# Performance work log

Measured on AMD Instinct MI355X. Metric: run time of the kernel, lower is better.

The kernel has to match this reference:

```python
import jax, jax.numpy as jnp
import numpy as np


def setup_inputs() -> dict:
    key = jax.random.key(0)
    ks = jax.random.split(key, 8)
    B, N, M, H = 8192, 2048, 2048, 10
    return {
        "X": jax.random.normal(ks[0], (B, N), dtype=jnp.float32),
        "weight": jax.random.normal(ks[1], (N, M), dtype=jnp.float32),
        "W1": jax.random.normal(ks[2], (3, H), dtype=jnp.float32) * 0.5,
        "b1": jax.random.normal(ks[3], (H,), dtype=jnp.float32) * 0.1,
        "W2": jax.random.normal(ks[4], (H, H), dtype=jnp.float32) * 0.3,
        "b2": jax.random.normal(ks[5], (H,), dtype=jnp.float32) * 0.1,
        "W3": jax.random.normal(ks[6], (H, 1), dtype=jnp.float32) * 0.3,
        "b3": jax.random.normal(ks[7], (1,), dtype=jnp.float32) * 0.1,
    }


def reference(X, weight, W1, b1, W2, b2, W3, b3):
    # NCA local rule, vectorized over all (i, j) cells.
    # 'forward'  = mean of column j excluding row i  (leave-one-out col mean)
    # 'backward' = mean of row i excluding column j  (leave-one-out row mean)
    n, m = weight.shape
    col_sum = jnp.sum(weight, axis=0, keepdims=True)            # [1, m]
    row_sum = jnp.sum(weight, axis=1, keepdims=True)            # [n, 1]
    fwd_mean = (col_sum - weight) / jnp.float32(n - 1)          # [n, m]
    bwd_mean = (row_sum - weight) / jnp.float32(m - 1)          # [n, m]
    feats = jnp.stack([weight, fwd_mean, bwd_mean], axis=-1)    # [n, m, 3]
    # tiny 3 -> 10 -> 10 -> 1 MLP applied per cell
    h = jax.nn.relu(feats @ W1 + b1)                            # [n, m, 10]
    h = jax.nn.relu(h @ W2 + b2)                                # [n, m, 10]
    updates = (h @ W3 + b3)[..., 0]                             # [n, m]
    new_weight = weight + updates
    # forward: softmax(X @ W)
    return jax.nn.softmax(X @ new_weight, axis=-1)
```

## Files before the change

### kernel.cpp

```cpp
#include <hip/hip_runtime.h>
#include <hip/hip_bf16.h>


typedef int int4v __attribute__((ext_vector_type(4)));
typedef int int16v __attribute__((ext_vector_type(16)));

#define GK 2048
#define NROWS 2048
#define MCOLS 2048
#define NCHUNK 16

#define CS_BLOCKS 128
#define RS_BLOCKS 2048
__global__ __launch_bounds__(256) void pre_kernel(
    const float* __restrict__ X, const float* __restrict__ W,
    signed char* __restrict__ X1, signed char* __restrict__ X2,
    float* __restrict__ sx1,
    float* __restrict__ part, float* __restrict__ rowS) {
  const int bid = blockIdx.x;
  const int tid = threadIdx.x;

  if (bid < CS_BLOCKS) {
    int chunk = bid >> 3;
    int j = (bid & 7) * 256 + tid;
    int i0 = chunk * (NROWS / NCHUNK);
    float s = 0.f;
    for (int i = i0; i < i0 + NROWS / NCHUNK; ++i) s += W[(size_t)i * MCOLS + j];
    part[(size_t)chunk * MCOLS + j] = s;
    return;
  }
  if (bid < CS_BLOCKS + RS_BLOCKS) {
    int row = bid - CS_BLOCKS;
    const float4* p = (const float4*)(W + (size_t)row * MCOLS);
    float4 a = p[tid];
    float4 b = p[tid + 256];
    float v = (a.x + a.y) + (a.z + a.w) + (b.x + b.y) + (b.z + b.w);
    __shared__ float red[256];
    red[tid] = v;
    __syncthreads();
    for (int s = 128; s > 0; s >>= 1) {
      if (tid < s) red[tid] += red[tid + s];
      __syncthreads();
    }
    if (tid == 0) rowS[row] = red[0];
    return;
  }
  {
    int row = bid - CS_BLOCKS - RS_BLOCKS;
    const float4* xr = (const float4*)(X + (size_t)row * GK);
    float4 a = xr[tid * 2];
    float4 b = xr[tid * 2 + 1];
    float xs[8] = {a.x, a.y, a.z, a.w, b.x, b.y, b.z, b.w};
    float am = 0.f;
#pragma unroll
    for (int i = 0; i < 8; ++i) am = fmaxf(am, fabsf(xs[i]));
    const int lane = tid & 63, wv = tid >> 6;
#pragma unroll
    for (int off = 32; off > 0; off >>= 1)
      am = fmaxf(am, __shfl_xor(am, off));
    __shared__ float wred[4];
    if (lane == 0) wred[wv] = am;
    __syncthreads();
    float amax = fmaxf(fmaxf(wred[0], wred[1]), fmaxf(wred[2], wred[3]));
    float s1 = amax * (1.0f / 127.0f);
    float inv = 127.0f / amax;
    int q1[8], q2[8];
#pragma unroll
    for (int i = 0; i < 8; ++i) {
      q1[i] = (int)rintf(xs[i] * inv);
      float r = xs[i] - (float)q1[i] * s1;
      q2[i] = (int)rintf(r * (254.0f * inv));
    }
    unsigned lo1 = (q1[0] & 255) | ((q1[1] & 255) << 8) | ((q1[2] & 255) << 16) | ((q1[3] & 255) << 24);
    unsigned hi1 = (q1[4] & 255) | ((q1[5] & 255) << 8) | ((q1[6] & 255) << 16) | ((q1[7] & 255) << 24);
    unsigned lo2 = (q2[0] & 255) | ((q2[1] & 255) << 8) | ((q2[2] & 255) << 16) | ((q2[3] & 255) << 24);
    unsigned hi2 = (q2[4] & 255) | ((q2[5] & 255) << 8) | ((q2[6] & 255) << 16) | ((q2[7] & 255) << 24);
    ((uint2*)(X1 + (size_t)row * GK))[tid] = make_uint2(lo1, hi1);
    ((uint2*)(X2 + (size_t)row * GK))[tid] = make_uint2(lo2, hi2);
    if (tid == 0) sx1[row] = s1;
  }
}

__global__ __launch_bounds__(256) void nca_update_kernel(
    const float* __restrict__ W, const float* __restrict__ part,
    const float* __restrict__ rowS,
    const float* __restrict__ W1, const float* __restrict__ b1,
    const float* __restrict__ W2, const float* __restrict__ b2,
    const float* __restrict__ W3, const float* __restrict__ b3,
    float* __restrict__ Wt) {
  __shared__ float sColS[32];
  __shared__ float cred[NCHUNK][33];
  __shared__ float Tf[32][33];
  const int tid = threadIdx.x;
  const int i0 = blockIdx.y * 32;
  const int j0 = blockIdx.x * 32;

  {
    int ch = tid >> 5;
    int jl = tid & 31;
    cred[ch][jl]     = part[(size_t)ch * MCOLS + j0 + jl];
    cred[ch + 8][jl] = part[(size_t)(ch + 8) * MCOLS + j0 + jl];
  }
  __syncthreads();
  if (tid < 32) {
    float s = 0.f;
#pragma unroll
    for (int c = 0; c < NCHUNK; ++c) s += cred[c][tid];
    sColS[tid] = s;
  }
  __syncthreads();

  const int r = tid >> 5;
  const int c = tid & 31;

  float w[4], fwd[4], bwd[4];
#pragma unroll
  for (int cell = 0; cell < 4; ++cell) {
    int il = r + 8 * cell;
    float wv = W[(size_t)(i0 + il) * MCOLS + j0 + c];
    w[cell] = wv;
    fwd[cell] = (sColS[c] - wv) * (1.0f / (float)(NROWS - 1));
    bwd[cell] = (rowS[i0 + il] - wv) * (1.0f / (float)(MCOLS - 1));
  }

  float h1[4][10];
#pragma unroll
  for (int o = 0; o < 10; ++o) {
    float w1a = W1[o], w1b = W1[10 + o], w1c = W1[20 + o], bb = b1[o];
#pragma unroll
    for (int cell = 0; cell < 4; ++cell) {
      float v = fmaf(w[cell], w1a, fmaf(fwd[cell], w1b, fmaf(bwd[cell], w1c, bb)));
      h1[cell][o] = fmaxf(v, 0.f);
    }
  }
  const float b3v = b3[0];
  float u[4] = {b3v, b3v, b3v, b3v};
#pragma unroll
  for (int o = 0; o < 10; ++o) {
    float h2[4];
    float bb = b2[o];
#pragma unroll
    for (int cell = 0; cell < 4; ++cell) h2[cell] = bb;
#pragma unroll
    for (int p = 0; p < 10; ++p) {
      float wv = W2[p * 10 + o];
#pragma unroll
      for (int cell = 0; cell < 4; ++cell) h2[cell] = fmaf(h1[cell][p], wv, h2[cell]);
    }
    float w3 = W3[o];
#pragma unroll
    for (int cell = 0; cell < 4; ++cell) u[cell] = fmaf(fmaxf(h2[cell], 0.f), w3, u[cell]);
  }

#pragma unroll
  for (int cell = 0; cell < 4; ++cell) {
    int il = r + 8 * cell;
    Tf[il][c] = w[cell] + u[cell];
  }
  __syncthreads();

  {
    int r2 = tid >> 4;
    int ic = (tid & 15) * 2;
#pragma unroll
    for (int half = 0; half < 2; ++half) {
      int jl = r2 + 16 * half;
      float2 v = make_float2(Tf[ic][jl], Tf[ic + 1][jl]);
      *(float2*)(&Wt[(size_t)(j0 + jl) * NROWS + i0 + ic]) = v;
    }
  }
}

__global__ __launch_bounds__(256) void bquant_kernel(
    const float* __restrict__ Wt, signed char* __restrict__ B1,
    signed char* __restrict__ B2, float* __restrict__ sw1) {
  const int row = blockIdx.x;
  const int tid = threadIdx.x;
  const float4* wr = (const float4*)(Wt + (size_t)row * GK);
  float4 a = wr[tid * 2];
  float4 b = wr[tid * 2 + 1];
  float xs[8] = {a.x, a.y, a.z, a.w, b.x, b.y, b.z, b.w};
  float am = 0.f;
#pragma unroll
  for (int i = 0; i < 8; ++i) am = fmaxf(am, fabsf(xs[i]));
  const int lane = tid & 63, wv = tid >> 6;
#pragma unroll
  for (int off = 32; off > 0; off >>= 1)
    am = fmaxf(am, __shfl_xor(am, off));
  __shared__ float wred[4];
  if (lane == 0) wred[wv] = am;
  __syncthreads();
  float amax = fmaxf(fmaxf(wred[0], wred[1]), fmaxf(wred[2], wred[3]));
  float s1 = amax * (1.0f / 127.0f);
  float inv = 127.0f / amax;
  int q1[8], q2[8];
#pragma unroll
  for (int i = 0; i < 8; ++i) {
    q1[i] = (int)rintf(xs[i] * inv);
    float r = xs[i] - (float)q1[i] * s1;
    q2[i] = (int)rintf(r * (254.0f * inv));
  }
  unsigned lo1 = (q1[0] & 255) | ((q1[1] & 255) << 8) | ((q1[2] & 255) << 16) | ((q1[3] & 255) << 24);
  unsigned hi1 = (q1[4] & 255) | ((q1[5] & 255) << 8) | ((q1[6] & 255) << 16) | ((q1[7] & 255) << 24);
  unsigned lo2 = (q2[0] & 255) | ((q2[1] & 255) << 8) | ((q2[2] & 255) << 16) | ((q2[3] & 255) << 24);
  unsigned hi2 = (q2[4] & 255) | ((q2[5] & 255) << 8) | ((q2[6] & 255) << 16) | ((q2[7] & 255) << 24);
  ((uint2*)(B1 + (size_t)row * GK))[tid] = make_uint2(lo1, hi1);
  ((uint2*)(B2 + (size_t)row * GK))[tid] = make_uint2(lo2, hi2);
  if (tid == 0) sw1[row] = s1;
}

#define BM 128
#define BN 128
#define BK 64
#define NT (GK / BK)
#define BUFSZ 32768
#define SROWSZ ((size_t)16 * GK)

__device__ __forceinline__ void glds16(const signed char* g, char* l) {
  __builtin_amdgcn_global_load_lds(
      (const __attribute__((address_space(1))) void*)g,
      (__attribute__((address_space(3))) void*)l, 16, 0, 0);
}

__device__ __forceinline__ int4v ds_read128(const char* p) {
  int4v r;
  asm volatile("ds_read_b128 %0, %1"
               : "=v"(r)
               : "v"((const __attribute__((address_space(3))) char*)p));
  return r;
}

#define MFMA_I8 __builtin_amdgcn_mfma_i32_32x32x32_i8

#define RD16(NX, rb_)                                                          \
  NX##a1[0][0] = ds_read128((rb_) + aoff[0][0]);                               \
  NX##a1[0][1] = ds_read128((rb_) + aoff[0][1]);                               \
  NX##a1[1][0] = ds_read128((rb_) + aoff[1][0]);                               \
  NX##a1[1][1] = ds_read128((rb_) + aoff[1][1]);                               \
  NX##a2[0][0] = ds_read128((rb_) + aoff[0][0] + 8192);                        \
  NX##a2[0][1] = ds_read128((rb_) + aoff[0][1] + 8192);                        \
  NX##a2[1][0] = ds_read128((rb_) + aoff[1][0] + 8192);                        \
  NX##a2[1][1] = ds_read128((rb_) + aoff[1][1] + 8192);                        \
  NX##b1[0][0] = ds_read128((rb_) + boff[0][0]);                               \
  NX##b1[0][1] = ds_read128((rb_) + boff[0][1]);                               \
  NX##b1[1][0] = ds_read128((rb_) + boff[1][0]);                               \
  NX##b1[1][1] = ds_read128((rb_) + boff[1][1]);                               \
  NX##b2[0][0] = ds_read128((rb_) + boff[0][0] + 8192);                        \
  NX##b2[0][1] = ds_read128((rb_) + boff[0][1] + 8192);                        \
  NX##b2[1][0] = ds_read128((rb_) + boff[1][0] + 8192);                        \
  NX##b2[1][1] = ds_read128((rb_) + boff[1][1] + 8192);

#define MM12(CUR, ks)                                                          \
  acc_h[0][0] = MFMA_I8(CUR##a1[0][ks], CUR##b1[0][ks], acc_h[0][0], 0, 0, 0); \
  acc_h[0][1] = MFMA_I8(CUR##a1[0][ks], CUR##b1[1][ks], acc_h[0][1], 0, 0, 0); \
  acc_h[1][0] = MFMA_I8(CUR##a1[1][ks], CUR##b1[0][ks], acc_h[1][0], 0, 0, 0); \
  acc_h[1][1] = MFMA_I8(CUR##a1[1][ks], CUR##b1[1][ks], acc_h[1][1], 0, 0, 0); \
  acc_c[0][0] = MFMA_I8(CUR##a1[0][ks], CUR##b2[0][ks], acc_c[0][0], 0, 0, 0); \
  acc_c[0][1] = MFMA_I8(CUR##a1[0][ks], CUR##b2[1][ks], acc_c[0][1], 0, 0, 0); \
  acc_c[1][0] = MFMA_I8(CUR##a1[1][ks], CUR##b2[0][ks], acc_c[1][0], 0, 0, 0); \
  acc_c[1][1] = MFMA_I8(CUR##a1[1][ks], CUR##b2[1][ks], acc_c[1][1], 0, 0, 0); \
  acc_c[0][0] = MFMA_I8(CUR##a2[0][ks], CUR##b1[0][ks], acc_c[0][0], 0, 0, 0); \
  acc_c[0][1] = MFMA_I8(CUR##a2[0][ks], CUR##b1[1][ks], acc_c[0][1], 0, 0, 0); \
  acc_c[1][0] = MFMA_I8(CUR##a2[1][ks], CUR##b1[0][ks], acc_c[1][0], 0, 0, 0); \
  acc_c[1][1] = MFMA_I8(CUR##a2[1][ks], CUR##b1[1][ks], acc_c[1][1], 0, 0, 0);

#define STAGE8(wb_, gp_)                                                       \
  glds16((gp_) + 0 * SROWSZ, (wb_) + 0 * 1024 + lane * 16);                    \
  glds16((gp_) + 1 * SROWSZ, (wb_) + 1 * 1024 + lane * 16);                    \
  glds16((gp_) + 2 * SROWSZ, (wb_) + 2 * 1024 + lane * 16);                    \
  glds16((gp_) + 3 * SROWSZ, (wb_) + 3 * 1024 + lane * 16);                    \
  glds16((gp_) + 4 * SROWSZ, (wb_) + 4 * 1024 + lane * 16);                    \
  glds16((gp_) + 5 * SROWSZ, (wb_) + 5 * 1024 + lane * 16);                    \
  glds16((gp_) + 6 * SROWSZ, (wb_) + 6 * 1024 + lane * 16);                    \
  glds16((gp_) + 7 * SROWSZ, (wb_) + 7 * 1024 + lane * 16);

#define STEP(i, CUR, NXT)                                                      \
  {                                                                            \
    if ((i) + 2 < NT) asm volatile("s_waitcnt vmcnt(8)" ::: "memory");         \
    else              asm volatile("s_waitcnt vmcnt(0)" ::: "memory");         \
    __builtin_amdgcn_s_barrier();                                              \
    if ((i) + 1 < NT) {                                                        \
      const char* rb_ = sL + (((i) + 1) & 3) * BUFSZ;                          \
      RD16(NXT, rb_);                                                          \
    }                                                                          \
    if ((i) + 3 < NT) {                                                        \
      char* wb_ = sL + (((i) + 3) & 3) * BUFSZ + wave * 8192;                  \
      const signed char* gp_ = gw + (size_t)((i) + 3) * BK;                    \
      STAGE8(wb_, gp_);                                                        \
    }                                                                          \
    if ((i) + 1 < NT) asm volatile("s_waitcnt lgkmcnt(15)" ::: "memory");      \
    else              asm volatile("s_waitcnt lgkmcnt(0)" ::: "memory");       \
    __builtin_amdgcn_sched_barrier(0);                                         \
    __builtin_amdgcn_s_setprio(1);                                             \
    MM12(CUR, 0);                                                              \
    MM12(CUR, 1);                                                              \
    __builtin_amdgcn_s_setprio(0);                                             \
  }

__global__ __launch_bounds__(256, 1) void gemm_kernel(
    const signed char* __restrict__ X1, const signed char* __restrict__ X2,
    const signed char* __restrict__ B1, const signed char* __restrict__ B2,
    const float* __restrict__ sw1, float* __restrict__ C) {
  __shared__ __align__(16) char sL[4 * BUFSZ];

  const int tid = threadIdx.x;
  const int lane = tid & 63;
  const int wave = tid >> 6;
  const int wr = wave >> 1;
  const int wc = wave & 1;

  const int bx = blockIdx.x;
  const int by = blockIdx.y;

  const signed char* A1g = X1 + (size_t)(by * BM) * GK;
  const signed char* A2g = X2 + (size_t)(by * BM) * GK;
  const signed char* B1g = B1 + (size_t)(bx * BN) * GK;
  const signed char* B2g = B2 + (size_t)(bx * BN) * GK;

  const int srow = lane >> 2;
  const int schk = (lane & 3) ^ ((lane >> 3) & 3);
  const signed char* gw =
      (wave == 0 ? A1g : wave == 1 ? A2g : wave == 2 ? B1g : B2g) +
      (size_t)srow * GK + schk * 16;

  const int rl = lane & 15;
  const int fhalf = (lane >> 4) & 1;
  const int fck = lane >> 5;
  int aoff[2][2], boff[2][2];
#pragma unroll
  for (int mi = 0; mi < 2; ++mi)
#pragma unroll
    for (int ks = 0; ks < 2; ++ks) {
      int c = 2 * ks + fck;
      int slot = 4 * rl + (c ^ ((rl >> 1) & 3));
      aoff[mi][ks] = (wr * 4 + mi * 2 + fhalf) * 1024 + slot * 16;
      boff[mi][ks] = 16384 + (wc * 4 + mi * 2 + fhalf) * 1024 + slot * 16;
    }

  int16v acc_h[2][2], acc_c[2][2];
#pragma unroll
  for (int i = 0; i < 2; ++i)
#pragma unroll
    for (int j = 0; j < 2; ++j)
#pragma unroll
      for (int e = 0; e < 16; ++e) { acc_h[i][j][e] = 0; acc_c[i][j][e] = 0; }

  int4v s0_a1[2][2], s0_a2[2][2], s0_b1[2][2], s0_b2[2][2];
  int4v s1_a1[2][2], s1_a2[2][2], s1_b1[2][2], s1_b2[2][2];

#pragma unroll
  for (int t = 0; t < 3; ++t) {
    char* wb = sL + t * BUFSZ + wave * 8192;
    const signed char* gp = gw + (size_t)t * BK;
    STAGE8(wb, gp);
  }
  asm volatile("s_waitcnt vmcnt(16)" ::: "memory");
  __builtin_amdgcn_s_barrier();
  RD16(s0_, sL);

#pragma unroll 1
  for (int i = 0; i < NT; i += 2) {
    STEP(i, s0_, s1_);
    STEP(i + 1, s1_, s0_);
  }

  const int ecol = lane & 31;
  const int erow = 4 * (lane >> 5);
#pragma unroll
  for (int ni = 0; ni < 2; ++ni) {
    int col = bx * BN + wc * 64 + ni * 32 + ecol;
    float sw = sw1[col];
#pragma unroll
    for (int mi = 0; mi < 2; ++mi) {
#pragma unroll
      for (int reg = 0; reg < 16; ++reg) {
        int row = by * BM + wr * 64 + mi * 32 + (reg & 3) + 8 * (reg >> 2) + erow;
        float v = (float)acc_h[mi][ni][reg] + (float)acc_c[mi][ni][reg] * (1.0f / 254.0f);
        C[(size_t)row * MCOLS + col] = v * sw;
      }
    }
  }
}

__global__ __launch_bounds__(256) void softmax_kernel(
    float* __restrict__ C, const float* __restrict__ sx1) {
  const int lane = threadIdx.x & 63;
  const int wv = threadIdx.x >> 6;
  const int row = blockIdx.x * 4 + wv;
  const float sx = sx1[row];
  float4* p = (float4*)(C + (size_t)row * MCOLS);

  float4 v[8];
#pragma unroll
  for (int j = 0; j < 8; ++j) {
    v[j] = p[j * 64 + lane];
    v[j].x *= sx; v[j].y *= sx; v[j].z *= sx; v[j].w *= sx;
  }

  float vmax = -3.4e38f;
#pragma unroll
  for (int j = 0; j < 8; ++j)
    vmax = fmaxf(vmax, fmaxf(fmaxf(v[j].x, v[j].y), fmaxf(v[j].z, v[j].w)));
#pragma unroll
  for (int off = 32; off > 0; off >>= 1)
    vmax = fmaxf(vmax, __shfl_xor(vmax, off));

  float sum = 0.f;
#pragma unroll
  for (int j = 0; j < 8; ++j) {
    v[j].x = __expf(v[j].x - vmax);
    v[j].y = __expf(v[j].y - vmax);
    v[j].z = __expf(v[j].z - vmax);
    v[j].w = __expf(v[j].w - vmax);
    sum += (v[j].x + v[j].y) + (v[j].z + v[j].w);
  }
#pragma unroll
  for (int off = 32; off > 0; off >>= 1)
    sum += __shfl_xor(sum, off);
  float inv = 1.0f / sum;

#pragma unroll
  for (int j = 0; j < 8; ++j) {
    v[j].x *= inv; v[j].y *= inv; v[j].z *= inv; v[j].w *= inv;
    p[j * 64 + lane] = v[j];
  }
}

extern "C" void kernel_launch(void* const* d_in, const int* in_sizes, int n_in,
                              void* d_out, int out_size, void* d_ws, size_t ws_size,
                              hipStream_t stream) {
  const float* X      = (const float*)d_in[0];
  const float* weight = (const float*)d_in[1];
  const float* W1     = (const float*)d_in[2];
  const float* b1     = (const float*)d_in[3];
  const float* W2     = (const float*)d_in[4];
  const float* b2     = (const float*)d_in[5];
  const float* W3     = (const float*)d_in[6];
  const float* b3     = (const float*)d_in[7];
  float* out = (float*)d_out;

  const int N = 2048, M = 2048;
  const int Bdim = in_sizes[0] / N;

  float* rowS = (float*)d_ws;
  float* part = rowS + 2048;
  float* sx1  = part + NCHUNK * 2048;
  float* sw1  = sx1 + 8192;
  float* Wt   = sw1 + 2048;
  signed char* X1 = (signed char*)(Wt + (size_t)M * N);
  signed char* X2 = X1 + (size_t)Bdim * N;
  signed char* B1q = X2 + (size_t)Bdim * N;
  signed char* B2q = B1q + (size_t)M * N;

  pre_kernel<<<CS_BLOCKS + RS_BLOCKS + Bdim, 256, 0, stream>>>(
      X, weight, X1, X2, sx1, part, rowS);

  nca_update_kernel<<<dim3(M / 32, N / 32), 256, 0, stream>>>(
      weight, part, rowS, W1, b1, W2, b2, W3, b3, Wt);

  bquant_kernel<<<M, 256, 0, stream>>>(Wt, B1q, B2q, sw1);

  gemm_kernel<<<dim3(M / BN, Bdim / BM), 256, 0, stream>>>(
      X1, X2, B1q, B2q, sw1, out);

  softmax_kernel<<<Bdim / 4, 256, 0, stream>>>(out, sx1);
}
```

Measured before the change: 317.5 us.

## Load B fragments directly from global into registers, shrink LDS to A-only ring

The int8 GEMM mainloop no longer stages the B operands through LDS. Each wave loads its B1/B2 fragments straight from global memory into registers with global_load_dwordx4, double-buffered across iterations. Only the A operands go through a 3-stage LDS ring of 48KB instead of the 128KB 4-stage A+B buffer, and launch bounds allow 2 blocks per CU. The aim is to cut LDS traffic and footprint so occupancy can rise, at the cost of B data being fetched redundantly by both wave rows and of more complex vmcnt accounting.

```diff
diff --git a/kernel.cpp b/kernel.cpp
--- a/kernel.cpp
+++ b/kernel.cpp
@@ -213,8 +213,7 @@
 #define BN 128
 #define BK 64
 #define NT (GK / BK)
-#define BUFSZ 32768
-#define SROWSZ ((size_t)16 * GK)
+#define ABUF 16384
 
 __device__ __forceinline__ void glds16(const signed char* g, char* l) {
   __builtin_amdgcn_global_load_lds(
@@ -230,78 +229,76 @@
   return r;
 }
 
+#define GLOAD(dst, vo, base, off)                                              \
+  asm volatile("global_load_dwordx4 %0, %1, %2 offset:" off                    \
+               : "=v"(dst) : "v"(vo), "s"(base))
+
 #define MFMA_I8 __builtin_amdgcn_mfma_i32_32x32x32_i8
 
-#define RD16(NX, rb_)                                                          \
-  NX##a1[0][0] = ds_read128((rb_) + aoff[0][0]);                               \
-  NX##a1[0][1] = ds_read128((rb_) + aoff[0][1]);                               \
-  NX##a1[1][0] = ds_read128((rb_) + aoff[1][0]);                               \
-  NX##a1[1][1] = ds_read128((rb_) + aoff[1][1]);                               \
-  NX##a2[0][0] = ds_read128((rb_) + aoff[0][0] + 8192);                        \
-  NX##a2[0][1] = ds_read128((rb_) + aoff[0][1] + 8192);                        \
-  NX##a2[1][0] = ds_read128((rb_) + aoff[1][0] + 8192);                        \
-  NX##a2[1][1] = ds_read128((rb_) + aoff[1][1] + 8192);                        \
-  NX##b1[0][0] = ds_read128((rb_) + boff[0][0]);                               \
-  NX##b1[0][1] = ds_read128((rb_) + boff[0][1]);                               \
-  NX##b1[1][0] = ds_read128((rb_) + boff[1][0]);                               \
-  NX##b1[1][1] = ds_read128((rb_) + boff[1][1]);                               \
-  NX##b2[0][0] = ds_read128((rb_) + boff[0][0] + 8192);                        \
-  NX##b2[0][1] = ds_read128((rb_) + boff[0][1] + 8192);                        \
-  NX##b2[1][0] = ds_read128((rb_) + boff[1][0] + 8192);                        \
-  NX##b2[1][1] = ds_read128((rb_) + boff[1][1] + 8192);
+#define LOADB(NX)                                                              \
+  GLOAD(NX##b1[0][0], vb0, B1g, "0");  GLOAD(NX##b1[0][1], vb0, B1g, "32");    \
+  GLOAD(NX##b1[1][0], vb1, B1g, "0");  GLOAD(NX##b1[1][1], vb1, B1g, "32");    \
+  GLOAD(NX##b2[0][0], vb0, B2g, "0");  GLOAD(NX##b2[0][1], vb0, B2g, "32");    \
+  GLOAD(NX##b2[1][0], vb1, B2g, "0");  GLOAD(NX##b2[1][1], vb1, B2g, "32");    \
+  vb0 += 64; vb1 += 64;
+
+#define STAGEA(wb_, koff_)                                                     \
+  glds16(gA0 + (koff_), (wb_) + swb0);                                         \
+  glds16(gA1 + (koff_), (wb_) + swb1);                                         \
+  glds16(gA2 + (koff_), (wb_) + swb2);                                         \
+  glds16(gA3 + (koff_), (wb_) + swb3);
 
 #define MM12(CUR, ks)                                                          \
-  acc_h[0][0] = MFMA_I8(CUR##a1[0][ks], CUR##b1[0][ks], acc_h[0][0], 0, 0, 0); \
-  acc_h[0][1] = MFMA_I8(CUR##a1[0][ks], CUR##b1[1][ks], acc_h[0][1], 0, 0, 0); \
-  acc_h[1][0] = MFMA_I8(CUR##a1[1][ks], CUR##b1[0][ks], acc_h[1][0], 0, 0, 0); \
-  acc_h[1][1] = MFMA_I8(CUR##a1[1][ks], CUR##b1[1][ks], acc_h[1][1], 0, 0, 0); \
-  acc_c[0][0] = MFMA_I8(CUR##a1[0][ks], CUR##b2[0][ks], acc_c[0][0], 0, 0, 0); \
-  acc_c[0][1] = MFMA_I8(CUR##a1[0][ks], CUR##b2[1][ks], acc_c[0][1], 0, 0, 0); \
-  acc_c[1][0] = MFMA_I8(CUR##a1[1][ks], CUR##b2[0][ks], acc_c[1][0], 0, 0, 0); \
-  acc_c[1][1] = MFMA_I8(CUR##a1[1][ks], CUR##b2[1][ks], acc_c[1][1], 0, 0, 0); \
-  acc_c[0][0] = MFMA_I8(CUR##a2[0][ks], CUR##b1[0][ks], acc_c[0][0], 0, 0, 0); \
-  acc_c[0][1] = MFMA_I8(CUR##a2[0][ks], CUR##b1[1][ks], acc_c[0][1], 0, 0, 0); \
-  acc_c[1][0] = MFMA_I8(CUR##a2[1][ks], CUR##b1[0][ks], acc_c[1][0], 0, 0, 0); \
-  acc_c[1][1] = MFMA_I8(CUR##a2[1][ks], CUR##b1[1][ks], acc_c[1][1], 0, 0, 0);
-
-#define STAGE8(wb_, gp_)                                                       \
-  glds16((gp_) + 0 * SROWSZ, (wb_) + 0 * 1024 + lane * 16);                    \
-  glds16((gp_) + 1 * SROWSZ, (wb_) + 1 * 1024 + lane * 16);                    \
-  glds16((gp_) + 2 * SROWSZ, (wb_) + 2 * 1024 + lane * 16);                    \
-  glds16((gp_) + 3 * SROWSZ, (wb_) + 3 * 1024 + lane * 16);                    \
-  glds16((gp_) + 4 * SROWSZ, (wb_) + 4 * 1024 + lane * 16);                    \
-  glds16((gp_) + 5 * SROWSZ, (wb_) + 5 * 1024 + lane * 16);                    \
-  glds16((gp_) + 6 * SROWSZ, (wb_) + 6 * 1024 + lane * 16);                    \
-  glds16((gp_) + 7 * SROWSZ, (wb_) + 7 * 1024 + lane * 16);
+  acc_h[0][0] = MFMA_I8(a1f[0][ks], CUR##b1[0][ks], acc_h[0][0], 0, 0, 0);     \
+  acc_h[0][1] = MFMA_I8(a1f[0][ks], CUR##b1[1][ks], acc_h[0][1], 0, 0, 0);     \
+  acc_h[1][0] = MFMA_I8(a1f[1][ks], CUR##b1[0][ks], acc_h[1][0], 0, 0, 0);     \
+  acc_h[1][1] = MFMA_I8(a1f[1][ks], CUR##b1[1][ks], acc_h[1][1], 0, 0, 0);     \
+  acc_c[0][0] = MFMA_I8(a1f[0][ks], CUR##b2[0][ks], acc_c[0][0], 0, 0, 0);     \
+  acc_c[0][1] = MFMA_I8(a1f[0][ks], CUR##b2[1][ks], acc_c[0][1], 0, 0, 0);     \
+  acc_c[1][0] = MFMA_I8(a1f[1][ks], CUR##b2[0][ks], acc_c[1][0], 0, 0, 0);     \
+  acc_c[1][1] = MFMA_I8(a1f[1][ks], CUR##b2[1][ks], acc_c[1][1], 0, 0, 0);     \
+  acc_c[0][0] = MFMA_I8(a2f[0][ks], CUR##b1[0][ks], acc_c[0][0], 0, 0, 0);     \
+  acc_c[0][1] = MFMA_I8(a2f[0][ks], CUR##b1[1][ks], acc_c[0][1], 0, 0, 0);     \
+  acc_c[1][0] = MFMA_I8(a2f[1][ks], CUR##b1[0][ks], acc_c[1][0], 0, 0, 0);     \
+  acc_c[1][1] = MFMA_I8(a2f[1][ks], CUR##b1[1][ks], acc_c[1][1], 0, 0, 0);
 
 #define STEP(i, CUR, NXT)                                                      \
   {                                                                            \
-    if ((i) + 2 < NT) asm volatile("s_waitcnt vmcnt(8)" ::: "memory");         \
-    else              asm volatile("s_waitcnt vmcnt(0)" ::: "memory");         \
+    if ((i) == NT - 1) asm volatile("s_waitcnt vmcnt(8)" ::: "memory");        \
+    else               asm volatile("s_waitcnt vmcnt(12)" ::: "memory");       \
     __builtin_amdgcn_s_barrier();                                              \
-    if ((i) + 1 < NT) {                                                        \
-      const char* rb_ = sL + (((i) + 1) & 3) * BUFSZ;                          \
-      RD16(NXT, rb_);                                                          \
-    }                                                                          \
-    if ((i) + 3 < NT) {                                                        \
-      char* wb_ = sL + (((i) + 3) & 3) * BUFSZ + wave * 8192;                  \
-      const signed char* gp_ = gw + (size_t)((i) + 3) * BK;                    \
-      STAGE8(wb_, gp_);                                                        \
-    }                                                                          \
-    if ((i) + 1 < NT) asm volatile("s_waitcnt lgkmcnt(15)" ::: "memory");      \
-    else              asm volatile("s_waitcnt lgkmcnt(0)" ::: "memory");       \
+    __builtin_amdgcn_sched_barrier(0);                                         \
+    a1f[0][0] = ds_read128(rbuf + aoff[0][0]);                                 \
+    a1f[0][1] = ds_read128(rbuf + aoff[0][1]);                                 \
+    a1f[1][0] = ds_read128(rbuf + aoff[1][0]);                                 \
+    a1f[1][1] = ds_read128(rbuf + aoff[1][1]);                                 \
+    a2f[0][0] = ds_read128(rbuf + aoff[0][0] + 8192);                          \
+    a2f[0][1] = ds_read128(rbuf + aoff[0][1] + 8192);                          \
+    a2f[1][0] = ds_read128(rbuf + aoff[1][0] + 8192);                          \
+    a2f[1][1] = ds_read128(rbuf + aoff[1][1] + 8192);                          \
+    __builtin_amdgcn_sched_barrier(0);                                         \
+    if ((i) + 1 < NT) { LOADB(NXT); }                                          \
+    __builtin_amdgcn_sched_barrier(0);                                         \
+    if ((i) + 2 < NT) { STAGEA(wbuf, (size_t)((i) + 2) * BK); }                \
+    __builtin_amdgcn_sched_barrier(0);                                         \
+    asm volatile("s_waitcnt lgkmcnt(0)" ::: "memory");                         \
+    if ((i) < NT - 2)       asm volatile("s_waitcnt vmcnt(16)" ::: "memory");  \
+    else if ((i) == NT - 2) asm volatile("s_waitcnt vmcnt(12)" ::: "memory");  \
+    else                    asm volatile("s_waitcnt vmcnt(0)" ::: "memory");   \
     __builtin_amdgcn_sched_barrier(0);                                         \
     __builtin_amdgcn_s_setprio(1);                                             \
     MM12(CUR, 0);                                                              \
     MM12(CUR, 1);                                                              \
     __builtin_amdgcn_s_setprio(0);                                             \
-  }
-
-__global__ __launch_bounds__(256, 1) void gemm_kernel(
+    rbuf += ABUF; if (rbuf == sL + 3 * ABUF) rbuf = sL;                        \
+    wbuf += ABUF; if (wbuf == sL + 3 * ABUF) wbuf = sL;                        \
+  }
+
+__global__ __launch_bounds__(256, 2) void gemm_kernel(
     const signed char* __restrict__ X1, const signed char* __restrict__ X2,
-    const signed char* __restrict__ B1, const signed char* __restrict__ B2,
+    const signed char* __restrict__ B1q, const signed char* __restrict__ B2q,
     const float* __restrict__ sw1, float* __restrict__ C) {
-  __shared__ __align__(16) char sL[4 * BUFSZ];
+  __shared__ __align__(16) char sL[3 * ABUF];
 
   const int tid = threadIdx.x;
   const int lane = tid & 63;
@@ -314,19 +311,26 @@
 
   const signed char* A1g = X1 + (size_t)(by * BM) * GK;
   const signed char* A2g = X2 + (size_t)(by * BM) * GK;
-  const signed char* B1g = B1 + (size_t)(bx * BN) * GK;
-  const signed char* B2g = B2 + (size_t)(bx * BN) * GK;
+  const signed char* B1g = B1q + (size_t)(bx * BN) * GK;
+  const signed char* B2g = B2q + (size_t)(bx * BN) * GK;
 
   const int srow = lane >> 2;
   const int schk = (lane & 3) ^ ((lane >> 3) & 3);
-  const signed char* gw =
-      (wave == 0 ? A1g : wave == 1 ? A2g : wave == 2 ? B1g : B2g) +
-      (size_t)srow * GK + schk * 16;
+  const int b0 = wave * 4;
+  const signed char* gAbase = (b0 >= 8) ? A2g : A1g;
+  const signed char* gA0 = gAbase + (size_t)(((b0 + 0) & 7) * 16 + srow) * GK + schk * 16;
+  const signed char* gA1 = gAbase + (size_t)(((b0 + 1) & 7) * 16 + srow) * GK + schk * 16;
+  const signed char* gA2 = gAbase + (size_t)(((b0 + 2) & 7) * 16 + srow) * GK + schk * 16;
+  const signed char* gA3 = gAbase + (size_t)(((b0 + 3) & 7) * 16 + srow) * GK + schk * 16;
+  const int swb0 = (b0 + 0) * 1024;
+  const int swb1 = (b0 + 1) * 1024;
+  const int swb2 = (b0 + 2) * 1024;
+  const int swb3 = (b0 + 3) * 1024;
 
   const int rl = lane & 15;
   const int fhalf = (lane >> 4) & 1;
   const int fck = lane >> 5;
-  int aoff[2][2], boff[2][2];
+  int aoff[2][2];
 #pragma unroll
   for (int mi = 0; mi < 2; ++mi)
 #pragma unroll
@@ -334,8 +338,10 @@
       int c = 2 * ks + fck;
       int slot = 4 * rl + (c ^ ((rl >> 1) & 3));
       aoff[mi][ks] = (wr * 4 + mi * 2 + fhalf) * 1024 + slot * 16;
-      boff[mi][ks] = 16384 + (wc * 4 + mi * 2 + fhalf) * 1024 + slot * 16;
-    }
+    }
+
+  unsigned vb0 = (unsigned)((wc * 64 + (lane & 31)) * GK + ((lane >> 5) << 4));
+  unsigned vb1 = vb0 + 32u * GK;
 
   int16v acc_h[2][2], acc_c[2][2];
 #pragma unroll
@@ -345,18 +351,18 @@
 #pragma unroll
       for (int e = 0; e < 16; ++e) { acc_h[i][j][e] = 0; acc_c[i][j][e] = 0; }
 
-  int4v s0_a1[2][2], s0_a2[2][2], s0_b1[2][2], s0_b2[2][2];
-  int4v s1_a1[2][2], s1_a2[2][2], s1_b1[2][2], s1_b2[2][2];
-
-#pragma unroll
-  for (int t = 0; t < 3; ++t) {
-    char* wb = sL + t * BUFSZ + wave * 8192;
-    const signed char* gp = gw + (size_t)t * BK;
-    STAGE8(wb, gp);
-  }
-  asm volatile("s_waitcnt vmcnt(16)" ::: "memory");
-  __builtin_amdgcn_s_barrier();
-  RD16(s0_, sL);
+  int4v a1f[2][2], a2f[2][2];
+  int4v s0_b1[2][2], s0_b2[2][2], s1_b1[2][2], s1_b2[2][2];
+
+  const char* rbuf = sL;
+  char* wbuf = sL + 2 * ABUF;
+
+  STAGEA(sL, 0);
+  __builtin_amdgcn_sched_barrier(0);
+  LOADB(s0_);
+  __builtin_amdgcn_sched_barrier(0);
+  STAGEA(sL + ABUF, BK);
+  __builtin_amdgcn_sched_barrier(0);
 
 #pragma unroll 1
   for (int i = 0; i < NT; i += 2) {
```

Result: slower. 376.5 us (+18.6%).
